# Optimization experiments

Measured on AMD Instinct MI355X. Metric: run time of the kernel, lower is better.

Reference implementation:

```python
import jax, jax.numpy as jnp
import numpy as np

B, L = 1, 512
D_NODE, D_EDGE = 256, 128
H, DH, NQK, NV = 8, 48, 4, 8
INF, EPS = 1.0e6, 1.0e-6
CONCAT = D_EDGE // 4 + DH + NV * 4  # 112 per head


def _rope(x, pos):
    # standard rotate-half RoPE over head dim; x: [b,l,h,d], pos: [b,l] int
    half = x.shape[-1] // 2
    inv_freq = 1.0 / (10000.0 ** (jnp.arange(half, dtype=jnp.float32) / half))
    ang = pos[..., None].astype(jnp.float32) * inv_freq            # [b,l,half]
    cos, sin = jnp.cos(ang)[..., None, :], jnp.sin(ang)[..., None, :]
    x1, x2 = x[..., :half], x[..., half:]
    return jnp.concatenate([x1 * cos - x2 * sin, x1 * sin + x2 * cos], axis=-1)


def _split3(p):
    # torch.stack(torch.split(p, p.shape[-1]//3, -1), -1): [..., 3k] -> [..., k, 3]
    lead = p.shape[:-1]
    return jnp.swapaxes(p.reshape(lead + (3, p.shape[-1] // 3)), -1, -2)


def _forward(s, z, affines, node_pos, mask, Wq, bq, Wkv, bkv, Wqp, bqp,
             Wkvp, bkvp, Wb, bb, Wdown, bdown, head_weights, Wout, bout):
    b, l = s.shape[:2]
    rot = affines[..., :3, :3]                                     # [b,l,3,3]
    trans = affines[..., :3, 3]                                    # [b,l,3]

    q = (s @ Wq + bq).reshape(b, l, H, DH)
    kv = (s @ Wkv + bkv).reshape(b, l, H, 2 * DH)
    k, v = kv[..., :DH], kv[..., DH:]
    q, k = _rope(q, node_pos), _rope(k, node_pos)

    q_pts = _split3(s @ Wqp + bqp)                                 # [b,l,H*NQK,3]
    q_pts = jnp.einsum('blij,blpj->blpi', rot, q_pts) + trans[:, :, None, :]
    q_pts = q_pts.reshape(b, l, H, NQK, 3)
    kv_pts = _split3(s @ Wkvp + bkvp)                              # [b,l,H*(NQK+NV),3]
    kv_pts = jnp.einsum('blij,blpj->blpi', rot, kv_pts) + trans[:, :, None, :]
    kv_pts = kv_pts.reshape(b, l, H, NQK + NV, 3)
    k_pts, v_pts = kv_pts[..., :NQK, :], kv_pts[..., NQK:, :]

    bias = z @ Wb + bb                                             # [b,l,m,H]
    a = jnp.einsum('blhd,bmhd->bhlm', q, k) * np.sqrt(1.0 / (3 * DH))
    a = a + np.sqrt(1.0 / 3) * jnp.transpose(bias, (0, 3, 1, 2))

    disp = q_pts[:, :, None] - k_pts[:, None]                      # [b,l,m,H,NQK,3]
    d2 = jnp.sum(disp * disp, axis=-1)                             # [b,l,m,H,NQK]
    hw = jax.nn.softplus(head_weights) * np.sqrt(1.0 / (3 * (NQK * 9.0 / 2)))
    pt_att = -0.5 * jnp.sum(d2 * hw[:, None], axis=-1)             # [b,l,m,H]
    a = a + jnp.transpose(pt_att, (0, 3, 1, 2))

    sq_mask = INF * (mask[:, :, None] * mask[:, None, :] - 1.0)    # [b,l,m]
    a = jax.nn.softmax(a + sq_mask[:, None], axis=-1)              # [b,H,l,m]

    o = jnp.einsum('bhlm,bmhd->blhd', a, v).reshape(b, l, H * DH)
    o_pt = jnp.einsum('bhlm,bmhpc->blhpc', a, v_pts)               # [b,l,H,NV,3]
    o_pt = jnp.einsum('blji,blhpj->blhpi', rot, o_pt - trans[:, :, None, None, :])
    o_pt_norm = jnp.sqrt(jnp.sum(o_pt * o_pt, axis=-1) + EPS).reshape(b, l, H * NV)
    o_pt = o_pt.reshape(b, l, H * NV, 3)
    pair_z = z @ Wdown + bdown                                     # [b,l,m,D_EDGE//4]
    o_pair = jnp.einsum('bhlm,blmd->blhd', a, pair_z).reshape(b, l, -1)

    feats = jnp.concatenate([o, o_pt[..., 0], o_pt[..., 1], o_pt[..., 2],
                             o_pt_norm, o_pair], axis=-1)          # [b,l,H*CONCAT]
    return feats @ Wout + bout


def setup_inputs():
    key = jax.random.key(0)
    ks = jax.random.split(key, 12)

    def lin(i, din, dout):
        return (jax.random.normal(ks[i], (din, dout), jnp.float32) / np.sqrt(din),
                jnp.zeros((dout,), jnp.float32))

    Wq, bq = lin(2, D_NODE, H * DH)
    Wkv, bkv = lin(3, D_NODE, 2 * H * DH)
    Wqp, bqp = lin(4, D_NODE, H * NQK * 3)
    Wkvp, bkvp = lin(5, D_NODE, H * (NQK + NV) * 3)
    Wb, bb = lin(6, D_EDGE, H)
    Wdown, bdown = lin(7, D_EDGE, D_EDGE // 4)
    Wout, bout = lin(8, H * CONCAT, D_NODE)
    return {
        's': jax.random.normal(ks[0], (B, L, D_NODE), jnp.float32),
        'z': jax.random.normal(ks[1], (B, L, L, D_EDGE), jnp.float32),
        'affines': jax.random.normal(ks[9], (B, L, 3, 4), jnp.float32),
        'node_pos': jnp.broadcast_to(jnp.arange(L, dtype=jnp.int32), (B, L)),
        'mask': jnp.ones((B, L), jnp.float32),
        'Wq': Wq, 'bq': bq, 'Wkv': Wkv, 'bkv': bkv,
        'Wqp': Wqp, 'bqp': bqp, 'Wkvp': Wkvp, 'bkvp': bkvp,
        'Wb': Wb, 'bb': bb, 'Wdown': Wdown, 'bdown': bdown,
        'head_weights': jnp.full((H,), 0.541324854612918, jnp.float32),
        'Wout': Wout, 'bout': bout,
    }


def reference(s, z, affines, node_pos, mask, Wq, bq, Wkv, bkv, Wqp, bqp,
              Wkvp, bkvp, Wb, bb, Wdown, bdown, head_weights, Wout, bout):
    return _forward(s, z, affines, node_pos, mask, Wq, bq, Wkv, bkv, Wqp, bqp,
                    Wkvp, bkvp, Wb, bb, Wdown, bdown, head_weights, Wout, bout)
```

## Files before the change

kernel.cpp:

```cpp
#include <hip/hip_runtime.h>
#include <math.h>

#define LSEQ   512
#define DNODE  256
#define DEDGE  128
#define NH     8
#define DHD    48
#define NQKP   4
#define NVP    8

constexpr size_t N_RAW = (size_t)LSEQ*1536;
constexpr size_t N_QRO = (size_t)NH*LSEQ*DHD;
constexpr size_t N_KT  = (size_t)NH*DHD*LSEQ;
constexpr size_t N_VW  = (size_t)NH*LSEQ*DHD;
constexpr size_t N_QPW = (size_t)NH*LSEQ*12;
constexpr size_t N_KPT = (size_t)NH*12*LSEQ;
constexpr size_t N_VPT = (size_t)NH*LSEQ*24;
constexpr size_t N_BIA = (size_t)NH*LSEQ*LSEQ;
constexpr size_t N_PZ  = (size_t)LSEQ*LSEQ*32;
constexpr size_t N_AW  = (size_t)NH*LSEQ*LSEQ;
constexpr size_t N_OW  = (size_t)NH*LSEQ*DHD;
constexpr size_t N_OPT = (size_t)NH*LSEQ*24;
constexpr size_t N_OPR = (size_t)LSEQ*256;
constexpr size_t N_WT  = (size_t)40*128;

constexpr size_t OFF_RAW = 0;
constexpr size_t OFF_QRO = OFF_RAW + N_RAW;
constexpr size_t OFF_KT  = OFF_QRO + N_QRO;
constexpr size_t OFF_VW  = OFF_KT  + N_KT;
constexpr size_t OFF_QPW = OFF_VW  + N_VW;
constexpr size_t OFF_KPT = OFF_QPW + N_QPW;
constexpr size_t OFF_VPT = OFF_KPT + N_KPT;
constexpr size_t OFF_BIA = OFF_VPT + N_VPT;
constexpr size_t OFF_PZ  = OFF_BIA + N_BIA;
constexpr size_t OFF_AW  = OFF_PZ  + N_PZ;
constexpr size_t OFF_OW  = OFF_AW  + N_AW;
constexpr size_t OFF_OPT = OFF_OW  + N_OW;
constexpr size_t OFF_OPR = OFF_OPT + N_OPT;
constexpr size_t OFF_WT  = OFF_OPR + N_OPR;

__global__ __launch_bounds__(256) void k_proj(
    const float* __restrict__ s,
    const float* __restrict__ Wq,  const float* __restrict__ bq,
    const float* __restrict__ Wkv, const float* __restrict__ bkv,
    const float* __restrict__ Wqp, const float* __restrict__ bqp,
    const float* __restrict__ Wkvp,const float* __restrict__ bkvp,
    float* __restrict__ raw)
{
    __shared__ float s_lds[8][DNODE];
    int t  = threadIdx.x;
    int l0 = blockIdx.x * 8;
    const float4* sg = (const float4*)(s + (size_t)l0*DNODE);
    float4* sl = (float4*)(&s_lds[0][0]);
    sl[t]       = sg[t];
    sl[t + 256] = sg[t + 256];
    __syncthreads();

    const float* Wp[6]; int str[6]; float bv[6];
#pragma unroll
    for (int j = 0; j < 6; j++) {
        int o = t + 256*j;
        if (o < 384)        { Wp[j] = Wq  + o;        str[j] = 384; bv[j] = bq[o]; }
        else if (o < 1152)  { Wp[j] = Wkv + (o-384);  str[j] = 768; bv[j] = bkv[o-384]; }
        else if (o < 1248)  { Wp[j] = Wqp + (o-1152); str[j] = 96;  bv[j] = bqp[o-1152]; }
        else                { Wp[j] = Wkvp+ (o-1248); str[j] = 288; bv[j] = bkvp[o-1248]; }
    }
    float acc[6][8];
#pragma unroll
    for (int j = 0; j < 6; j++)
#pragma unroll
        for (int li = 0; li < 8; li++) acc[j][li] = 0.f;

    for (int c = 0; c < DNODE; c++) {
        float sv[8];
#pragma unroll
        for (int li = 0; li < 8; li++) sv[li] = s_lds[li][c];
#pragma unroll
        for (int j = 0; j < 6; j++) {
            float w = Wp[j][c * str[j]];
#pragma unroll
            for (int li = 0; li < 8; li++) acc[j][li] += sv[li] * w;
        }
    }
#pragma unroll
    for (int j = 0; j < 6; j++) {
        int o = t + 256*j;
#pragma unroll
        for (int li = 0; li < 8; li++)
            raw[(size_t)(l0+li)*1536 + o] = acc[j][li] + bv[j];
    }
}

__global__ __launch_bounds__(64) void k_post(
    const float* __restrict__ raw,
    const float* __restrict__ affines,
    const int*   __restrict__ node_pos,
    float* __restrict__ qro, float* __restrict__ kt, float* __restrict__ vw,
    float* __restrict__ qpw, float* __restrict__ kpt, float* __restrict__ vpt)
{
    int l = blockIdx.x, lane = threadIdx.x;
    float rot[3][3], tr[3];
#pragma unroll
    for (int i = 0; i < 3; i++) {
#pragma unroll
        for (int j = 0; j < 3; j++) rot[i][j] = affines[l*12 + i*4 + j];
        tr[i] = affines[l*12 + i*4 + 3];
    }
    float pos = (float)node_pos[l];
    const float* r = raw + (size_t)l*1536;

#pragma unroll
    for (int it = 0; it < 6; it++) {
        int pi  = lane + it*64;
        bool isq = pi < 192;
        int pk = isq ? pi : pi - 192;
        int h = pk / 24, i = pk % 24;
        float invf = powf(10000.f, -(float)i / 24.f);
        float ang = pos * invf;
        float sn, cs; sincosf(ang, &sn, &cs);
        if (isq) {
            float x1 = r[h*48 + i], x2 = r[h*48 + 24 + i];
            qro[((size_t)h*LSEQ + l)*48 + i]      = x1*cs - x2*sn;
            qro[((size_t)h*LSEQ + l)*48 + 24 + i] = x1*sn + x2*cs;
        } else {
            float x1 = r[384 + h*96 + i], x2 = r[384 + h*96 + 24 + i];
            kt[((size_t)h*48 + i)*LSEQ + l]      = x1*cs - x2*sn;
            kt[((size_t)h*48 + 24 + i)*LSEQ + l] = x1*sn + x2*cs;
        }
    }
#pragma unroll
    for (int it = 0; it < 6; it++) {
        int e = lane + it*64;
        int h = e / 48, d = e % 48;
        vw[((size_t)h*LSEQ + l)*48 + d] = r[384 + h*96 + 48 + d];
    }
    if (lane < 32) {
        int p = lane, h = p / 4, pk2 = p % 4;
        float pj[3];
#pragma unroll
        for (int j = 0; j < 3; j++) pj[j] = r[1152 + j*32 + p];
#pragma unroll
        for (int i = 0; i < 3; i++) {
            float x = rot[i][0]*pj[0] + rot[i][1]*pj[1] + rot[i][2]*pj[2] + tr[i];
            qpw[((size_t)h*LSEQ + l)*12 + pk2*3 + i] = x;
        }
    }
#pragma unroll
    for (int it = 0; it < 2; it++) {
        int p = lane + it*64;
        if (p < 96) {
            int h = p / 12, pp = p % 12;
            float pj[3];
#pragma unroll
            for (int j = 0; j < 3; j++) pj[j] = r[1248 + j*96 + p];
#pragma unroll
            for (int i = 0; i < 3; i++) {
                float x = rot[i][0]*pj[0] + rot[i][1]*pj[1] + rot[i][2]*pj[2] + tr[i];
                if (pp < 4) kpt[((size_t)h*12 + pp*3 + i)*LSEQ + l] = x;
                else        vpt[((size_t)h*LSEQ + l)*24 + (pp-4)*3 + i] = x;
            }
        }
    }
}

__global__ __launch_bounds__(256) void k_wprep(
    const float* __restrict__ Wb, const float* __restrict__ Wdown,
    float* __restrict__ wt)
{
    int t = threadIdx.x;
#pragma unroll
    for (int i = 0; i < 20; i++) {
        int idx = t + i*256;
        int o = idx >> 7, c = idx & 127;
        wt[idx] = (o < 8) ? Wb[c*8 + o] : Wdown[c*32 + (o - 8)];
    }
}

__global__ __launch_bounds__(256) void k_zproj(
    const float* __restrict__ z, const float* __restrict__ wt,
    const float* __restrict__ bb, const float* __restrict__ bdown,
    float* __restrict__ bias, float* __restrict__ pz)
{
    __shared__ float pls[2][64][41];
    int t = threadIdx.x, lane = t & 63, w = t >> 6;
    int mgroup = w >> 1;
    int half = __builtin_amdgcn_readfirstlane(w & 1);
    int l = blockIdx.y;
    int m = blockIdx.x*128 + mgroup*64 + lane;

    const float* zr_g = z + ((size_t)l*LSEQ + m)*DEDGE + half*64;
    float4 zr[16];
#pragma unroll
    for (int cc = 0; cc < 16; cc++) zr[cc] = ((const float4*)zr_g)[cc];

    float acc[40];
    const float* wh = wt + half*64;
#pragma unroll 4
    for (int o = 0; o < 40; o++) {
        const float4* wp = (const float4*)(wh + o*128);
        float a = 0.f;
#pragma unroll
        for (int cc = 0; cc < 16; cc++) {
            float4 w4 = wp[cc];
            float4 z4 = zr[cc];
            a += z4.x*w4.x + z4.y*w4.y + z4.z*w4.z + z4.w*w4.w;
        }
        acc[o] = a;
    }

    if (half == 1) {
#pragma unroll
        for (int o = 0; o < 40; o++) pls[mgroup][lane][o] = acc[o];
    }
    __syncthreads();
    if (half == 0) {
#pragma unroll
        for (int o = 0; o < 40; o++) acc[o] += pls[mgroup][lane][o];

#pragma unroll
        for (int o = 0; o < 8; o++)
            bias[((size_t)o*LSEQ + l)*LSEQ + m] = acc[o] + bb[o];
        float* pzr = pz + ((size_t)l*LSEQ + m)*32;
#pragma unroll
        for (int o = 0; o < 32; o += 4) {
            float4 v4 = make_float4(acc[8+o]   + bdown[o],
                                    acc[8+o+1] + bdown[o+1],
                                    acc[8+o+2] + bdown[o+2],
                                    acc[8+o+3] + bdown[o+3]);
            *(float4*)(pzr + o) = v4;
        }
    }
}

__global__ __launch_bounds__(256) void k_logits(
    const float* __restrict__ qro, const float* __restrict__ kt,
    const float* __restrict__ qpw, const float* __restrict__ kpt,
    const float* __restrict__ bias, const float* __restrict__ mask,
    const float* __restrict__ head_weights,
    float* __restrict__ aw)
{
    __shared__ float qs[4][48];
    __shared__ float qps[4][12];
    int t = threadIdx.x, w = t >> 6, lane = t & 63;
    int idx = blockIdx.x*4 + w;
    int h = idx >> 9, l = idx & 511;

    if (lane < 48)      qs[w][lane]       = qro[((size_t)h*LSEQ + l)*48 + lane];
    else if (lane < 60) qps[w][lane - 48] = qpw[((size_t)h*LSEQ + l)*12 + (lane - 48)];
    __syncthreads();

    float hw = log1pf(__expf(head_weights[h])) * 0.13608276348795434f;
    float maskl = mask[l];

    float acc[8], d2a[8];
#pragma unroll
    for (int r2 = 0; r2 < 8; r2++) { acc[r2] = 0.f; d2a[r2] = 0.f; }

    for (int d = 0; d < 48; d++) {
        float qv = qs[w][d];
        const float* kp = kt + ((size_t)h*48 + d)*LSEQ + lane;
#pragma unroll
        for (int r2 = 0; r2 < 8; r2++) acc[r2] += qv * kp[r2*64];
    }
#pragma unroll
    for (int cmp = 0; cmp < 12; cmp++) {
        float qp = qps[w][cmp];
        const float* kp = kpt + ((size_t)h*12 + cmp)*LSEQ + lane;
#pragma unroll
        for (int r2 = 0; r2 < 8; r2++) { float df = qp - kp[r2*64]; d2a[r2] += df*df; }
    }
    float lg[8]; float mx = -1e30f;
#pragma unroll
    for (int r2 = 0; r2 < 8; r2++) {
        int m = lane + r2*64;
        float b  = bias[((size_t)h*LSEQ + l)*LSEQ + m];
        float mm = mask[m];
        lg[r2] = acc[r2]*(1.f/12.f) + 0.57735026919f*b - 0.5f*hw*d2a[r2]
               + 1000000.f*(maskl*mm - 1.f);
        mx = fmaxf(mx, lg[r2]);
    }
#pragma unroll
    for (int off = 32; off >= 1; off >>= 1) mx = fmaxf(mx, __shfl_xor(mx, off, 64));
    float sm = 0.f; float ex[8];
#pragma unroll
    for (int r2 = 0; r2 < 8; r2++) { ex[r2] = __expf(lg[r2] - mx); sm += ex[r2]; }
#pragma unroll
    for (int off = 32; off >= 1; off >>= 1) sm += __shfl_xor(sm, off, 64);
    float inv = 1.f / sm;
#pragma unroll
    for (int r2 = 0; r2 < 8; r2++)
        aw[((size_t)h*LSEQ + l)*LSEQ + lane + r2*64] = ex[r2]*inv;
}

__global__ __launch_bounds__(256) void k_ov(
    const float* __restrict__ aw, const float* __restrict__ vw,
    const float* __restrict__ vpt,
    float* __restrict__ ow, float* __restrict__ opt)
{
    __shared__ float as[4][LSEQ];
    int t = threadIdx.x, w = t >> 6, lane = t & 63;
    int idx = blockIdx.x*4 + w;
    int h = idx >> 9, l = idx & 511;

    const float* ar = aw + ((size_t)h*LSEQ + l)*LSEQ;
#pragma unroll
    for (int r2 = 0; r2 < 8; r2++) as[w][lane + r2*64] = ar[lane + r2*64];
    __syncthreads();

    const float* p0; int s0;
    if (lane < 48) { p0 = vw  + (size_t)h*LSEQ*48 + lane;        s0 = 48; }
    else           { p0 = vpt + (size_t)h*LSEQ*24 + (lane - 48); s0 = 24; }
    int o1 = (lane < 8) ? (16 + lane) : 16;
    const float* p1 = vpt + (size_t)h*LSEQ*24 + o1;

    float acc0 = 0.f, acc1 = 0.f;
    for (int m = 0; m < LSEQ; m++) {
        float av = as[w][m];
        acc0 += av * p0[(size_t)m*s0];
        acc1 += av * p1[(size_t)m*24];
    }
    if (lane < 48) ow[((size_t)h*LSEQ + l)*48 + lane] = acc0;
    else           opt[((size_t)h*LSEQ + l)*24 + (lane - 48)] = acc0;
    if (lane < 8)  opt[((size_t)h*LSEQ + l)*24 + 16 + lane]   = acc1;
}

__global__ __launch_bounds__(256) void k_opair(
    const float* __restrict__ aw, const float* __restrict__ pz,
    float* __restrict__ opr)
{
    __shared__ float as[NH][LSEQ];
    int t = threadIdx.x;
    int l = blockIdx.x;
    int hh = t >> 5, mb = t & 31;
#pragma unroll
    for (int r2 = 0; r2 < 16; r2++)
        as[hh][mb + r2*32] = aw[((size_t)hh*LSEQ + l)*LSEQ + mb + r2*32];
    __syncthreads();

    int d = t & 31, h = t >> 5;
    float acc = 0.f;
    const float* pzb = pz + (size_t)l*LSEQ*32 + d;
    for (int m = 0; m < LSEQ; m++) acc += as[h][m] * pzb[(size_t)m*32];
    opr[(size_t)l*256 + t] = acc;
}

__global__ __launch_bounds__(256) void k_final(
    const float* __restrict__ ow, const float* __restrict__ opt,
    const float* __restrict__ opr, const float* __restrict__ affines,
    const float* __restrict__ Wout, const float* __restrict__ bout,
    float* __restrict__ out)
{
    __shared__ float fs[4][896];
    int t = threadIdx.x;
    int l0 = blockIdx.x * 4;
#pragma unroll
    for (int li = 0; li < 4; li++) {
        int l = l0 + li;
        for (int e = t; e < 384; e += 256) {
            int h = e / 48, d = e % 48;
            fs[li][e] = ow[((size_t)h*LSEQ + l)*48 + d];
        }
        if (t < 64) {
            int h = t >> 3, p = t & 7;
            const float* ob = opt + ((size_t)h*LSEQ + l)*24 + p*3;
            float r0 = ob[0], r1 = ob[1], r2v = ob[2];
            float tr0 = affines[l*12 + 3], tr1 = affines[l*12 + 7], tr2 = affines[l*12 + 11];
            float x0 = r0 - tr0, x1 = r1 - tr1, x2 = r2v - tr2;
            float o0 = affines[l*12+0]*x0 + affines[l*12+4]*x1 + affines[l*12+8]*x2;
            float o1 = affines[l*12+1]*x0 + affines[l*12+5]*x1 + affines[l*12+9]*x2;
            float o2 = affines[l*12+2]*x0 + affines[l*12+6]*x1 + affines[l*12+10]*x2;
            fs[li][384 + t] = o0;
            fs[li][448 + t] = o1;
            fs[li][512 + t] = o2;
            fs[li][576 + t] = sqrtf(o0*o0 + o1*o1 + o2*o2 + 1e-6f);
        }
        fs[li][640 + t] = opr[(size_t)l*256 + t];
    }
    __syncthreads();

    float acc[4];
#pragma unroll
    for (int li = 0; li < 4; li++) acc[li] = bout[t];
    for (int c = 0; c < 896; c++) {
        float wv = Wout[(size_t)c*256 + t];
#pragma unroll
        for (int li = 0; li < 4; li++) acc[li] += fs[li][c] * wv;
    }
#pragma unroll
    for (int li = 0; li < 4; li++)
        out[(size_t)(l0 + li)*256 + t] = acc[li];
}

extern "C" void kernel_launch(void* const* d_in, const int* in_sizes, int n_in,
                              void* d_out, int out_size, void* d_ws, size_t ws_size,
                              hipStream_t stream)
{
    const float* s        = (const float*)d_in[0];
    const float* z        = (const float*)d_in[1];
    const float* affines  = (const float*)d_in[2];
    const int*   node_pos = (const int*)  d_in[3];
    const float* mask     = (const float*)d_in[4];
    const float* Wq   = (const float*)d_in[5];   const float* bq   = (const float*)d_in[6];
    const float* Wkv  = (const float*)d_in[7];   const float* bkv  = (const float*)d_in[8];
    const float* Wqp  = (const float*)d_in[9];   const float* bqp  = (const float*)d_in[10];
    const float* Wkvp = (const float*)d_in[11];  const float* bkvp = (const float*)d_in[12];
    const float* Wb   = (const float*)d_in[13];  const float* bb   = (const float*)d_in[14];
    const float* Wdown= (const float*)d_in[15];  const float* bdown= (const float*)d_in[16];
    const float* head_weights = (const float*)d_in[17];
    const float* Wout = (const float*)d_in[18];  const float* bout = (const float*)d_in[19];

    float* ws  = (float*)d_ws;
    float* raw = ws + OFF_RAW;
    float* qro = ws + OFF_QRO;
    float* kt  = ws + OFF_KT;
    float* vw  = ws + OFF_VW;
    float* qpw = ws + OFF_QPW;
    float* kpt = ws + OFF_KPT;
    float* vpt = ws + OFF_VPT;
    float* bia = ws + OFF_BIA;
    float* pz  = ws + OFF_PZ;
    float* aw  = ws + OFF_AW;
    float* owp = ws + OFF_OW;
    float* opt = ws + OFF_OPT;
    float* opr = ws + OFF_OPR;
    float* wt  = ws + OFF_WT;

    k_wprep<<<1, 256, 0, stream>>>(Wb, Wdown, wt);
    k_proj<<<64, 256, 0, stream>>>(s, Wq, bq, Wkv, bkv, Wqp, bqp, Wkvp, bkvp, raw);
    k_post<<<LSEQ, 64, 0, stream>>>(raw, affines, node_pos, qro, kt, vw, qpw, kpt, vpt);
    k_zproj<<<dim3(4, LSEQ), 256, 0, stream>>>(z, wt, bb, bdown, bia, pz);
    k_logits<<<1024, 256, 0, stream>>>(qro, kt, qpw, kpt, bia, mask, head_weights, aw);
    k_ov<<<1024, 256, 0, stream>>>(aw, vw, vpt, owp, opt);
    k_opair<<<LSEQ, 256, 0, stream>>>(aw, pz, opr);
    k_final<<<128, 256, 0, stream>>>(owp, opt, opr, affines, Wout, bout, (float*)d_out);
}
```

Measured before the change: 561.7 us.

## Fuse logits with attention-value pass and widen grids of projection and output kernels

Merges the logits/softmax kernel with the value-aggregation kernel so attention probabilities go into shared memory directly, avoiding a global re-read of the attention matrix. The node projection, post-processing and final output kernels are re-gridded to use many more blocks with less work per thread (768, 512x4, 512 blocks), trading register-level reuse of weights for occupancy. RoPE frequencies use exp2f instead of powf, and several loops get unroll pragmas. The smaller per-thread tiles re-read weights more often from global memory.

Measured after the change: 517.1 us. -7.9%, faster.

```diff
diff --git a/kernel.cpp b/kernel.cpp
--- a/kernel.cpp
+++ b/kernel.cpp
@@ -47,48 +47,34 @@
     const float* __restrict__ Wkvp,const float* __restrict__ bkvp,
     float* __restrict__ raw)
 {
-    __shared__ float s_lds[8][DNODE];
+    __shared__ float s_lds[4][DNODE];
     int t  = threadIdx.x;
-    int l0 = blockIdx.x * 8;
+    int l0 = (blockIdx.x / 6) * 4;
+    int o  = (blockIdx.x % 6) * 256 + t;
+
     const float4* sg = (const float4*)(s + (size_t)l0*DNODE);
-    float4* sl = (float4*)(&s_lds[0][0]);
-    sl[t]       = sg[t];
-    sl[t + 256] = sg[t + 256];
+    ((float4*)&s_lds[0][0])[t] = sg[t];
     __syncthreads();
 
-    const float* Wp[6]; int str[6]; float bv[6];
-#pragma unroll
-    for (int j = 0; j < 6; j++) {
-        int o = t + 256*j;
-        if (o < 384)        { Wp[j] = Wq  + o;        str[j] = 384; bv[j] = bq[o]; }
-        else if (o < 1152)  { Wp[j] = Wkv + (o-384);  str[j] = 768; bv[j] = bkv[o-384]; }
-        else if (o < 1248)  { Wp[j] = Wqp + (o-1152); str[j] = 96;  bv[j] = bqp[o-1152]; }
-        else                { Wp[j] = Wkvp+ (o-1248); str[j] = 288; bv[j] = bkvp[o-1248]; }
-    }
-    float acc[6][8];
-#pragma unroll
-    for (int j = 0; j < 6; j++)
-#pragma unroll
-        for (int li = 0; li < 8; li++) acc[j][li] = 0.f;
-
+    const float* Wp; int str; float bv;
+    if (o < 384)       { Wp = Wq   + o;        str = 384; bv = bq[o]; }
+    else if (o < 1152) { Wp = Wkv  + (o-384);  str = 768; bv = bkv[o-384]; }
+    else if (o < 1248) { Wp = Wqp  + (o-1152); str = 96;  bv = bqp[o-1152]; }
+    else               { Wp = Wkvp + (o-1248); str = 288; bv = bkvp[o-1248]; }
+
+    float a0 = 0.f, a1 = 0.f, a2 = 0.f, a3 = 0.f;
+#pragma unroll 8
     for (int c = 0; c < DNODE; c++) {
-        float sv[8];
-#pragma unroll
-        for (int li = 0; li < 8; li++) sv[li] = s_lds[li][c];
-#pragma unroll
-        for (int j = 0; j < 6; j++) {
-            float w = Wp[j][c * str[j]];
-#pragma unroll
-            for (int li = 0; li < 8; li++) acc[j][li] += sv[li] * w;
-        }
-    }
-#pragma unroll
-    for (int j = 0; j < 6; j++) {
-        int o = t + 256*j;
-#pragma unroll
-        for (int li = 0; li < 8; li++)
-            raw[(size_t)(l0+li)*1536 + o] = acc[j][li] + bv[j];
-    }
+        float w = Wp[(size_t)c * str];
+        a0 += s_lds[0][c] * w;
+        a1 += s_lds[1][c] * w;
+        a2 += s_lds[2][c] * w;
+        a3 += s_lds[3][c] * w;
+    }
+    raw[(size_t)(l0+0)*1536 + o] = a0 + bv;
+    raw[(size_t)(l0+1)*1536 + o] = a1 + bv;
+    raw[(size_t)(l0+2)*1536 + o] = a2 + bv;
+    raw[(size_t)(l0+3)*1536 + o] = a3 + bv;
 }
 
 __global__ __launch_bounds__(64) void k_post(
@@ -98,66 +84,73 @@
     float* __restrict__ qro, float* __restrict__ kt, float* __restrict__ vw,
     float* __restrict__ qpw, float* __restrict__ kpt, float* __restrict__ vpt)
 {
-    int l = blockIdx.x, lane = threadIdx.x;
-    float rot[3][3], tr[3];
-#pragma unroll
-    for (int i = 0; i < 3; i++) {
-#pragma unroll
-        for (int j = 0; j < 3; j++) rot[i][j] = affines[l*12 + i*4 + j];
-        tr[i] = affines[l*12 + i*4 + 3];
-    }
-    float pos = (float)node_pos[l];
+    int l = blockIdx.x, part = blockIdx.y, lane = threadIdx.x;
     const float* r = raw + (size_t)l*1536;
 
-#pragma unroll
-    for (int it = 0; it < 6; it++) {
-        int pi  = lane + it*64;
-        bool isq = pi < 192;
-        int pk = isq ? pi : pi - 192;
-        int h = pk / 24, i = pk % 24;
-        float invf = powf(10000.f, -(float)i / 24.f);
-        float ang = pos * invf;
-        float sn, cs; sincosf(ang, &sn, &cs);
-        if (isq) {
+    if (part == 0) {
+        float pos = (float)node_pos[l];
+#pragma unroll
+        for (int it = 0; it < 3; it++) {
+            int pk = lane + it*64;
+            int h = pk / 24, i = pk % 24;
+            float ang = pos * exp2f((float)i * -0.5536546825f);
+            float sn, cs; sincosf(ang, &sn, &cs);
             float x1 = r[h*48 + i], x2 = r[h*48 + 24 + i];
             qro[((size_t)h*LSEQ + l)*48 + i]      = x1*cs - x2*sn;
             qro[((size_t)h*LSEQ + l)*48 + 24 + i] = x1*sn + x2*cs;
-        } else {
+        }
+    } else if (part == 1) {
+        float pos = (float)node_pos[l];
+#pragma unroll
+        for (int it = 0; it < 3; it++) {
+            int pk = lane + it*64;
+            int h = pk / 24, i = pk % 24;
+            float ang = pos * exp2f((float)i * -0.5536546825f);
+            float sn, cs; sincosf(ang, &sn, &cs);
             float x1 = r[384 + h*96 + i], x2 = r[384 + h*96 + 24 + i];
             kt[((size_t)h*48 + i)*LSEQ + l]      = x1*cs - x2*sn;
             kt[((size_t)h*48 + 24 + i)*LSEQ + l] = x1*sn + x2*cs;
         }
-    }
-#pragma unroll
-    for (int it = 0; it < 6; it++) {
-        int e = lane + it*64;
-        int h = e / 48, d = e % 48;
-        vw[((size_t)h*LSEQ + l)*48 + d] = r[384 + h*96 + 48 + d];
-    }
-    if (lane < 32) {
-        int p = lane, h = p / 4, pk2 = p % 4;
-        float pj[3];
-#pragma unroll
-        for (int j = 0; j < 3; j++) pj[j] = r[1152 + j*32 + p];
+    } else if (part == 2) {
+#pragma unroll
+        for (int it = 0; it < 6; it++) {
+            int e = lane + it*64;
+            int h = e / 48, d = e % 48;
+            vw[((size_t)h*LSEQ + l)*48 + d] = r[384 + h*96 + 48 + d];
+        }
+    } else {
+        float rot[3][3], tr[3];
 #pragma unroll
         for (int i = 0; i < 3; i++) {
-            float x = rot[i][0]*pj[0] + rot[i][1]*pj[1] + rot[i][2]*pj[2] + tr[i];
-            qpw[((size_t)h*LSEQ + l)*12 + pk2*3 + i] = x;
-        }
-    }
-#pragma unroll
-    for (int it = 0; it < 2; it++) {
-        int p = lane + it*64;
-        if (p < 96) {
-            int h = p / 12, pp = p % 12;
+#pragma unroll
+            for (int j = 0; j < 3; j++) rot[i][j] = affines[l*12 + i*4 + j];
+            tr[i] = affines[l*12 + i*4 + 3];
+        }
+        if (lane < 32) {
+            int p = lane, h = p / 4, pk2 = p % 4;
             float pj[3];
 #pragma unroll
-            for (int j = 0; j < 3; j++) pj[j] = r[1248 + j*96 + p];
+            for (int j = 0; j < 3; j++) pj[j] = r[1152 + j*32 + p];
 #pragma unroll
             for (int i = 0; i < 3; i++) {
                 float x = rot[i][0]*pj[0] + rot[i][1]*pj[1] + rot[i][2]*pj[2] + tr[i];
-                if (pp < 4) kpt[((size_t)h*12 + pp*3 + i)*LSEQ + l] = x;
-                else        vpt[((size_t)h*LSEQ + l)*24 + (pp-4)*3 + i] = x;
+                qpw[((size_t)h*LSEQ + l)*12 + pk2*3 + i] = x;
+            }
+        }
+#pragma unroll
+        for (int it = 0; it < 2; it++) {
+            int p = lane + it*64;
+            if (p < 96) {
+                int h = p / 12, pp = p % 12;
+                float pj[3];
+#pragma unroll
+                for (int j = 0; j < 3; j++) pj[j] = r[1248 + j*96 + p];
+#pragma unroll
+                for (int i = 0; i < 3; i++) {
+                    float x = rot[i][0]*pj[0] + rot[i][1]*pj[1] + rot[i][2]*pj[2] + tr[i];
+                    if (pp < 4) kpt[((size_t)h*12 + pp*3 + i)*LSEQ + l] = x;
+                    else        vpt[((size_t)h*LSEQ + l)*24 + (pp-4)*3 + i] = x;
+                }
             }
         }
     }
@@ -232,13 +225,15 @@
     }
 }
 
-__global__ __launch_bounds__(256) void k_logits(
+__global__ __launch_bounds__(256) void k_attn(
     const float* __restrict__ qro, const float* __restrict__ kt,
     const float* __restrict__ qpw, const float* __restrict__ kpt,
     const float* __restrict__ bias, const float* __restrict__ mask,
     const float* __restrict__ head_weights,
-    float* __restrict__ aw)
-{
+    const float* __restrict__ vw, const float* __restrict__ vpt,
+    float* __restrict__ aw, float* __restrict__ ow, float* __restrict__ opt)
+{
+    __shared__ float as[4][LSEQ];
     __shared__ float qs[4][48];
     __shared__ float qps[4][12];
     int t = threadIdx.x, w = t >> 6, lane = t & 63;
@@ -256,6 +251,7 @@
 #pragma unroll
     for (int r2 = 0; r2 < 8; r2++) { acc[r2] = 0.f; d2a[r2] = 0.f; }
 
+#pragma unroll 4
     for (int d = 0; d < 48; d++) {
         float qv = qs[w][d];
         const float* kp = kt + ((size_t)h*48 + d)*LSEQ + lane;
@@ -288,25 +284,11 @@
     for (int off = 32; off >= 1; off >>= 1) sm += __shfl_xor(sm, off, 64);
     float inv = 1.f / sm;
 #pragma unroll
-    for (int r2 = 0; r2 < 8; r2++)
-        aw[((size_t)h*LSEQ + l)*LSEQ + lane + r2*64] = ex[r2]*inv;
-}
-
-__global__ __launch_bounds__(256) void k_ov(
-    const float* __restrict__ aw, const float* __restrict__ vw,
-    const float* __restrict__ vpt,
-    float* __restrict__ ow, float* __restrict__ opt)
-{
-    __shared__ float as[4][LSEQ];
-    int t = threadIdx.x, w = t >> 6, lane = t & 63;
-    int idx = blockIdx.x*4 + w;
-    int h = idx >> 9, l = idx & 511;
-
-    const float* ar = aw + ((size_t)h*LSEQ + l)*LSEQ;
-#pragma unroll
-    for (int r2 = 0; r2 < 8; r2++) as[w][lane + r2*64] = ar[lane + r2*64];
-    __syncthreads();
-
+    for (int r2 = 0; r2 < 8; r2++) {
+        float p = ex[r2]*inv;
+        aw[((size_t)h*LSEQ + l)*LSEQ + lane + r2*64] = p;
+        as[w][lane + r2*64] = p;
+    }
     const float* p0; int s0;
     if (lane < 48) { p0 = vw  + (size_t)h*LSEQ*48 + lane;        s0 = 48; }
     else           { p0 = vpt + (size_t)h*LSEQ*24 + (lane - 48); s0 = 24; }
@@ -314,6 +296,7 @@
     const float* p1 = vpt + (size_t)h*LSEQ*24 + o1;
 
     float acc0 = 0.f, acc1 = 0.f;
+#pragma unroll 8
     for (int m = 0; m < LSEQ; m++) {
         float av = as[w][m];
         acc0 += av * p0[(size_t)m*s0];
@@ -340,6 +323,7 @@
     int d = t & 31, h = t >> 5;
     float acc = 0.f;
     const float* pzb = pz + (size_t)l*LSEQ*32 + d;
+#pragma unroll 8
     for (int m = 0; m < LSEQ; m++) acc += as[h][m] * pzb[(size_t)m*32];
     opr[(size_t)l*256 + t] = acc;
 }
@@ -350,45 +334,36 @@
     const float* __restrict__ Wout, const float* __restrict__ bout,
     float* __restrict__ out)
 {
-    __shared__ float fs[4][896];
+    __shared__ float fs[896];
     int t = threadIdx.x;
-    int l0 = blockIdx.x * 4;
-#pragma unroll
-    for (int li = 0; li < 4; li++) {
-        int l = l0 + li;
-        for (int e = t; e < 384; e += 256) {
-            int h = e / 48, d = e % 48;
-            fs[li][e] = ow[((size_t)h*LSEQ + l)*48 + d];
-        }
-        if (t < 64) {
-            int h = t >> 3, p = t & 7;
-            const float* ob = opt + ((size_t)h*LSEQ + l)*24 + p*3;
-            float r0 = ob[0], r1 = ob[1], r2v = ob[2];
-            float tr0 = affines[l*12 + 3], tr1 = affines[l*12 + 7], tr2 = affines[l*12 + 11];
-            float x0 = r0 - tr0, x1 = r1 - tr1, x2 = r2v - tr2;
-            float o0 = affines[l*12+0]*x0 + affines[l*12+4]*x1 + affines[l*12+8]*x2;
-            float o1 = affines[l*12+1]*x0 + affines[l*12+5]*x1 + affines[l*12+9]*x2;
-            float o2 = affines[l*12+2]*x0 + affines[l*12+6]*x1 + affines[l*12+10]*x2;
-            fs[li][384 + t] = o0;
-            fs[li][448 + t] = o1;
-            fs[li][512 + t] = o2;
-            fs[li][576 + t] = sqrtf(o0*o0 + o1*o1 + o2*o2 + 1e-6f);
-        }
-        fs[li][640 + t] = opr[(size_t)l*256 + t];
-    }
+    int l = blockIdx.x;
+
+    for (int e = t; e < 384; e += 256) {
+        int h = e / 48, d = e % 48;
+        fs[e] = ow[((size_t)h*LSEQ + l)*48 + d];
+    }
+    if (t < 64) {
+        int h = t >> 3, p = t & 7;
+        const float* ob = opt + ((size_t)h*LSEQ + l)*24 + p*3;
+        float r0 = ob[0], r1 = ob[1], r2v = ob[2];
+        float tr0 = affines[l*12 + 3], tr1 = affines[l*12 + 7], tr2 = affines[l*12 + 11];
+        float x0 = r0 - tr0, x1 = r1 - tr1, x2 = r2v - tr2;
+        float o0 = affines[l*12+0]*x0 + affines[l*12+4]*x1 + affines[l*12+8]*x2;
+        float o1 = affines[l*12+1]*x0 + affines[l*12+5]*x1 + affines[l*12+9]*x2;
+        float o2 = affines[l*12+2]*x0 + affines[l*12+6]*x1 + affines[l*12+10]*x2;
+        fs[384 + t] = o0;
+        fs[448 + t] = o1;
+        fs[512 + t] = o2;
+        fs[576 + t] = sqrtf(o0*o0 + o1*o1 + o2*o2 + 1e-6f);
+    }
+    fs[640 + t] = opr[(size_t)l*256 + t];
     __syncthreads();
 
-    float acc[4];
-#pragma unroll
-    for (int li = 0; li < 4; li++) acc[li] = bout[t];
-    for (int c = 0; c < 896; c++) {
-        float wv = Wout[(size_t)c*256 + t];
-#pragma unroll
-        for (int li = 0; li < 4; li++) acc[li] += fs[li][c] * wv;
-    }
-#pragma unroll
-    for (int li = 0; li < 4; li++)
-        out[(size_t)(l0 + li)*256 + t] = acc[li];
+    float acc = bout[t];
+#pragma unroll 8
+    for (int c = 0; c < 896; c++)
+        acc += fs[c] * Wout[(size_t)c*256 + t];
+    out[(size_t)l*256 + t] = acc;
 }
 
 extern "C" void kernel_launch(void* const* d_in, const int* in_sizes, int n_in,
@@ -426,11 +401,11 @@
     float* wt  = ws + OFF_WT;
 
     k_wprep<<<1, 256, 0, stream>>>(Wb, Wdown, wt);
-    k_proj<<<64, 256, 0, stream>>>(s, Wq, bq, Wkv, bkv, Wqp, bqp, Wkvp, bkvp, raw);
-    k_post<<<LSEQ, 64, 0, stream>>>(raw, affines, node_pos, qro, kt, vw, qpw, kpt, vpt);
+    k_proj<<<768, 256, 0, stream>>>(s, Wq, bq, Wkv, bkv, Wqp, bqp, Wkvp, bkvp, raw);
+    k_post<<<dim3(LSEQ, 4), 64, 0, stream>>>(raw, affines, node_pos, qro, kt, vw, qpw, kpt, vpt);
     k_zproj<<<dim3(4, LSEQ), 256, 0, stream>>>(z, wt, bb, bdown, bia, pz);
-    k_logits<<<1024, 256, 0, stream>>>(qro, kt, qpw, kpt, bia, mask, head_weights, aw);
-    k_ov<<<1024, 256, 0, stream>>>(aw, vw, vpt, owp, opt);
+    k_attn<<<1024, 256, 0, stream>>>(qro, kt, qpw, kpt, bia, mask, head_weights,
+                                     vw, vpt, aw, owp, opt);
     k_opair<<<LSEQ, 256, 0, stream>>>(aw, pz, opr);
-    k_final<<<128, 256, 0, stream>>>(owp, opt, opr, affines, Wout, bout, (float*)d_out);
-}
+    k_final<<<512, 256, 0, stream>>>(owp, opt, opr, affines, Wout, bout, (float*)d_out);
+}
```
